# Optimization experiments

Hardware: AMD Instinct MI355X
Metric: run time of the kernel (lower is better)

## Reference

```python
import jax, jax.numpy as jnp
import numpy as np

BS, LS, NWRD, D, H, NTGT, MC = 32, 512, 100000, 128, 512, 2048, 20
TEMP = 0.5  # gumbel-softmax temperature (self.last_t)
HLOSS_COEF = 0.03


def setup_inputs() -> dict:
    key = jax.random.key(0)
    ks = jax.random.split(key, 12)
    inp_word = jax.random.randint(ks[0], (BS, LS), 0, NWRD, dtype=jnp.int32)
    inp_char = jax.random.randint(ks[1], (BS, LS, MC), 0, 95, dtype=jnp.int32)
    inp_pos = jax.random.randint(ks[2], (BS, LS), 0, 50, dtype=jnp.int32)
    keyword_table = jax.random.bernoulli(ks[3], 0.1, (NWRD,))  # wid in keywords_set
    tgt_ids = jax.random.randint(ks[4], (NTGT,), 0, NWRD, dtype=jnp.int32)
    lut = jax.random.randint(ks[5], (NWRD, MC), 0, 95, dtype=jnp.int32)
    u = jax.random.uniform(ks[6], (BS, LS, NTGT), minval=1e-6, maxval=1.0 - 1e-6)
    gumbel = -jnp.log(-jnp.log(u))  # standard Gumbel(0,1) noise
    W = jax.random.normal(ks[7], (NWRD, D), dtype=jnp.float32) * 0.02
    W1 = jax.random.normal(ks[8], (D, H), dtype=jnp.float32) * (1.0 / np.sqrt(D))
    b1 = jnp.zeros((H,), jnp.float32)
    W2 = jax.random.normal(ks[9], (H, NTGT), dtype=jnp.float32) * (1.0 / np.sqrt(H))
    b2 = jnp.zeros((NTGT,), jnp.float32)
    return dict(inp_word=inp_word, inp_char=inp_char, inp_pos=inp_pos,
                keyword_table=keyword_table, tgt_ids=tgt_ids, lut=lut,
                gumbel=gumbel, W=W, W1=W1, b1=b1, W2=W2, b2=b2)


def reference(inp_word, inp_char, inp_pos, keyword_table, tgt_ids, lut,
              gumbel, W, W1, b1, W2, b2):
    # keyword membership mask (idx in the original; torch gathers only masked
    # spots -- here we compute densely and select with the mask, same math at
    # every masked position, identity elsewhere)
    mask = keyword_table[inp_word]                      # [bs, ls] bool

    x = W[inp_word]                                     # embed: [bs, ls, d]
    hdn = jax.nn.relu(jnp.einsum('bsd,dh->bsh', x, W1) + b1)
    logits = jnp.einsum('bsh,ht->bst', hdn, W2) + b2    # [bs, ls, ntgt]

    # log_p.masked_scatter_(idx, x.max(-1)[0])
    log_p = jnp.where(mask, logits.max(axis=-1), 0.0)

    # hloss: mean entropy over masked spots * 0.03
    lsm = jax.nn.log_softmax(logits, axis=-1)
    ent = -jnp.sum(jnp.exp(lsm) * lsm, axis=-1)         # [bs, ls]
    n_spots = jnp.maximum(mask.sum(), 1)
    loss_h = (ent * mask).sum() / n_spots * HLOSS_COEF

    # gumbel_softmax(x, t): softmax((logits + g) / t)
    sft = jax.nn.softmax((logits + gumbel) / TEMP, axis=-1)  # [bs, ls, ntgt]

    # hard pick mapped through tgtwords, scattered into word
    y = tgt_ids[jnp.argmax(sft, axis=-1)]               # [bs, ls]
    word = jnp.where(mask, y, inp_word)

    # soft embedding: sft @ word_emb_tgt, word_emb_tgt = W[tgt_ids]
    x_emb = jnp.einsum('bst,td->bsd', sft, W[tgt_ids])  # [bs, ls, d]
    word_emb = jnp.where(mask[..., None], x_emb, x)     # scatter into W[word]

    char = lut[word]                                    # word_to_char lookup

    return (mask.astype(jnp.float32), log_p, word, char, word_emb, loss_h)
```

## Files before the change

kernel.cpp:

```cpp
#include <hip/hip_runtime.h>
#include <cstdint>

#define R_TOT 16384
#define T_NT  2048
#define DD    128
#define HH    512
#define MC_   20
#define BR    32
#define STEPS 64
#define NBLK  (R_TOT / BR)

#define MASK_OFF 0
#define LOGP_OFF 16384
#define WORD_OFF 32768
#define CHAR_OFF 49152
#define EMB_OFF  376832
#define LOSS_OFF 2473984

#define X_OFF     0
#define HDN_OFF   2097152
#define HDNB_OFF  10485760
#define WT_OFF    14680064
#define WTT4_OFF  14942208
#define W2T_OFF   15204352
#define W2P_OFF   16252928
#define ENT_OFF   16777216
#define CNT_OFF   16777728

typedef __attribute__((ext_vector_type(8))) short short8v;
typedef __attribute__((ext_vector_type(4))) float f32x4;
typedef unsigned short ushort_t;

__device__ __forceinline__ ushort_t f2bf(float f) {
    union { float f; unsigned int u; } v; v.f = f;
    unsigned int r = v.u + 0x7FFFu + ((v.u >> 16) & 1u);
    return (ushort_t)(r >> 16);
}

__device__ __forceinline__ void stage16(const ushort_t* gsrc, ushort_t* ldst) {
    __builtin_amdgcn_global_load_lds(
        (const __attribute__((address_space(1))) unsigned int*)gsrc,
        (__attribute__((address_space(3))) unsigned int*)ldst, 16, 0, 0);
}

__global__ __launch_bounds__(256) void k1_gather(
    const int* __restrict__ inp_word, const int* __restrict__ tgt_ids,
    const float* __restrict__ W, float* __restrict__ x, float* __restrict__ wtgt)
{
    int row = blockIdx.x * 2 + (threadIdx.x >> 7);
    int d = threadIdx.x & 127;
    if (row < R_TOT) {
        int wsrc = inp_word[row];
        x[(size_t)row * DD + d] = W[(size_t)wsrc * DD + d];
    } else {
        int rr = row - R_TOT;
        if (rr < T_NT) {
            int wsrc = tgt_ids[rr];
            wtgt[(size_t)rr * DD + d] = W[(size_t)wsrc * DD + d];
        }
    }
}

__global__ __launch_bounds__(256) void k1b_wtgtT4(
    const float* __restrict__ wtgt, ushort_t* __restrict__ wtgtT4)
{
    const int js = blockIdx.x, t = threadIdx.x;
    #pragma unroll
    for (int i = 0; i < 4; ++i) {
        int s = i * 256 + t;
        int cs = s >> 9, rem = s & 511;
        int df = rem >> 6, lane = rem & 63;
        int lrow = lane & 15, kg = lane >> 4;
        ushort_t* dst = wtgtT4 + (size_t)(((js * 2 + cs) * 8 + df) * 512 + lane * 8);
        #pragma unroll
        for (int j = 0; j < 8; ++j) {
            dst[j] = (j < 4)
                ? f2bf(wtgt[(size_t)(js * 32 + cs * 16 + kg * 4 + j) * DD + df * 16 + lrow])
                : (ushort_t)0;
        }
    }
}

__global__ __launch_bounds__(256) void k0_w2t(
    const float* __restrict__ W2, float* __restrict__ W2Tf, ushort_t* __restrict__ W2p)
{
    __shared__ float tile[32][33];
    const int js = blockIdx.x, ks = blockIdx.y;
    const int cb = js * 32, kb = ks * 32;
    const int lx = threadIdx.x & 31, ly = threadIdx.x >> 5;
    #pragma unroll
    for (int i = 0; i < 32; i += 8)
        tile[ly + i][lx] = W2[(size_t)(kb + ly + i) * T_NT + cb + lx];
    __syncthreads();
    #pragma unroll
    for (int i = 0; i < 32; i += 8) {
        int c = cb + ly + i, k = kb + lx;
        W2Tf[(size_t)c * HH + k] = tile[lx][ly + i];
    }
    if (threadIdx.x < 128) {
        int c = threadIdx.x >> 2, kgrp = threadIdx.x & 3;
        ushort_t* dst = W2p + (size_t)((js * 16 + ks) * 1024 + (c * 4 + kgrp) * 8);
        #pragma unroll
        for (int i = 0; i < 8; ++i)
            dst[i] = f2bf(tile[kgrp * 8 + i][c]);
    }
}

__global__ __launch_bounds__(256) void k2_hdn(
    const float* __restrict__ x, const float* __restrict__ W1,
    const float* __restrict__ b1, float* __restrict__ hdn, ushort_t* __restrict__ hdnB)
{
    __shared__ float As[16][64];
    __shared__ float Bs[16][64];
    const int t = threadIdx.x;
    const int bm = blockIdx.x * 64;
    const int bn = blockIdx.y * 64;
    const int tx = t & 15, ty = t >> 4;
    float acc[4][4] = {};
    for (int k0 = 0; k0 < DD; k0 += 16) {
        {
            int m = t >> 2, kq = t & 3;
            float4 v = *(const float4*)(x + (size_t)(bm + m) * DD + k0 + kq * 4);
            As[kq * 4 + 0][m] = v.x; As[kq * 4 + 1][m] = v.y;
            As[kq * 4 + 2][m] = v.z; As[kq * 4 + 3][m] = v.w;
        }
        {
            int k = t >> 4, nq = t & 15;
            *(float4*)(&Bs[k][nq * 4]) =
                *(const float4*)(W1 + (size_t)(k0 + k) * HH + bn + nq * 4);
        }
        __syncthreads();
        #pragma unroll
        for (int k = 0; k < 16; ++k) {
            float a[4], b[4];
            #pragma unroll
            for (int i = 0; i < 4; i++) a[i] = As[k][ty * 4 + i];
            #pragma unroll
            for (int j = 0; j < 4; j++) b[j] = Bs[k][tx * 4 + j];
            #pragma unroll
            for (int i = 0; i < 4; i++)
                #pragma unroll
                for (int j = 0; j < 4; j++)
                    acc[i][j] = fmaf(a[i], b[j], acc[i][j]);
        }
        __syncthreads();
    }
    #pragma unroll
    for (int i = 0; i < 4; i++) {
        int m = bm + ty * 4 + i;
        int n = bn + tx * 4;
        float4 v;
        v.x = fmaxf(acc[i][0] + b1[n + 0], 0.f);
        v.y = fmaxf(acc[i][1] + b1[n + 1], 0.f);
        v.z = fmaxf(acc[i][2] + b1[n + 2], 0.f);
        v.w = fmaxf(acc[i][3] + b1[n + 3], 0.f);
        *(float4*)(hdn + (size_t)m * HH + n) = v;
        ushort4 hb;
        hb.x = f2bf(v.x); hb.y = f2bf(v.y); hb.z = f2bf(v.z); hb.w = f2bf(v.w);
        *(ushort4*)(hdnB + (size_t)m * HH + n) = hb;
    }
}

__global__ __launch_bounds__(256) void k3_fused(
    const ushort_t* __restrict__ hdnB, const float* __restrict__ hdn,
    const ushort_t* __restrict__ W2p, const float* __restrict__ W2Tf,
    const float* __restrict__ b2, const float* __restrict__ gumbel,
    const int* __restrict__ inp_word, const int* __restrict__ keyword_table,
    const int* __restrict__ tgt_ids, const int* __restrict__ lut,
    const float* __restrict__ x, const ushort_t* __restrict__ wtgtT4,
    float* __restrict__ out, float* __restrict__ entP, float* __restrict__ cntP)
{
    __shared__ ushort_t wS[2 * 16384];
    __shared__ float statC1[32 * 8];
    __shared__ int   candS[BR * 2];
    __shared__ float invs2S[BR], entS[BR];
    __shared__ int   mskS[BR];

    const int t = threadIdx.x;
    const int wid = t >> 6, lane = t & 63;
    const int Mgrp = wid >> 1, Cgrp = wid & 1;
    const int lrow = lane & 15, kgrp = lane >> 4;
    const int row0 = blockIdx.x * BR;
    const int rowA = row0 + Mgrp * 16 + lrow;

    short8v av[16];
    #pragma unroll
    for (int ks = 0; ks < 16; ++ks)
        av[ks] = *(const short8v*)(hdnB + (size_t)rowA * HH + ks * 32 + kgrp * 8);

    const ushort_t* wb = wS + ((Cgrp * 16 + lrow) * 4 + kgrp) * 8;

    const float* gp = gumbel + (size_t)rowA * T_NT + Cgrp * 16 + kgrp * 4;
    const float* b2p = b2 + Cgrp * 16 + kgrp * 4;
    const ushort_t* vtp = wtgtT4 + (size_t)Cgrp * 4096 + lane * 8;

    float m_ = -1e30f, sE_ = 0.f, sEl_ = 0.f, s2_ = 0.f;
    float a1_ = -1e30f, a2_ = -1e30f;
    int i1_ = 0, i2_ = 0;
    f32x4 accpv[8];
    #pragma unroll
    for (int df = 0; df < 8; ++df) accpv[df] = (f32x4){0.f, 0.f, 0.f, 0.f};

    {
        const ushort_t* src = W2p + t * 8;
        ushort_t* dst = wS + t * 8;
        #pragma unroll
        for (int i = 0; i < 8; ++i) stage16(src + i * 2048, dst + i * 2048);
    }
    float4 g4 = *(const float4*)gp;
    float4 b2v4 = *(const float4*)b2p;
    __syncthreads();

    int c0 = Cgrp * 16 + kgrp * 4;

    for (int s = 0; s < STEPS; ++s) {
        const int buf = s & 1;

        if (s + 1 < STEPS) {
            const ushort_t* src = W2p + (size_t)(s + 1) * 16384 + t * 8;
            ushort_t* dst = wS + (buf ^ 1) * 16384 + t * 8;
            #pragma unroll
            for (int i = 0; i < 8; ++i) stage16(src + i * 2048, dst + i * 2048);
        }
        const int adv = (s + 1 < STEPS) ? 32 : 0;
        float4 gn4 = *(const float4*)(gp + adv);
        float4 b2n4 = *(const float4*)(b2p + adv);
        gp += 32; b2p += 32;
        short8v bvf[8];
        #pragma unroll
        for (int df = 0; df < 8; ++df)
            bvf[df] = *(const short8v*)(vtp + df * 512);
        vtp += 8192;

        const ushort_t* wbb = wb + buf * 16384;
        f32x4 ac0 = (f32x4){0.f,0.f,0.f,0.f}, ac1 = ac0, ac2 = ac0, ac3 = ac0;
        #pragma unroll
        for (int ks = 0; ks < 16; ks += 4) {
            ac0 = __builtin_amdgcn_mfma_f32_16x16x32_bf16(*(const short8v*)(wbb + (ks+0)*1024), av[ks+0], ac0, 0, 0, 0);
            ac1 = __builtin_amdgcn_mfma_f32_16x16x32_bf16(*(const short8v*)(wbb + (ks+1)*1024), av[ks+1], ac1, 0, 0, 0);
            ac2 = __builtin_amdgcn_mfma_f32_16x16x32_bf16(*(const short8v*)(wbb + (ks+2)*1024), av[ks+2], ac2, 0, 0, 0);
            ac3 = __builtin_amdgcn_mfma_f32_16x16x32_bf16(*(const short8v*)(wbb + (ks+3)*1024), av[ks+3], ac3, 0, 0, 0);
        }
        f32x4 acc = (ac0 + ac1) + (ac2 + ac3);

        short8v pav;
        pav[4] = 0; pav[5] = 0; pav[6] = 0; pav[7] = 0;
        #pragma unroll
        for (int q = 0; q < 4; ++q) {
            float l = acc[q] + b2v4[q];
            m_ = fmaxf(m_, l);
            float e1 = __expf(l);
            sE_ += e1; sEl_ = fmaf(e1, l, sEl_);
            float a = l + g4[q];
            float p = __expf(2.0f * a);
            s2_ += p;
            if (a > a1_) { a2_ = a1_; i2_ = i1_; a1_ = a; i1_ = c0 + q; }
            else if (a > a2_) { a2_ = a; i2_ = c0 + q; }
            pav[q] = (short)f2bf(p);
        }

        #pragma unroll
        for (int df = 0; df < 8; ++df)
            accpv[df] = __builtin_amdgcn_mfma_f32_16x16x32_bf16(pav, bvf[df], accpv[df], 0, 0, 0);

        g4 = gn4; b2v4 = b2n4; c0 += 32;
        __syncthreads();
    }

    #pragma unroll
    for (int mk = 16; mk < 64; mk <<= 1) {
        m_ = fmaxf(m_, __shfl_xor(m_, mk));
        sE_ += __shfl_xor(sE_, mk);
        sEl_ += __shfl_xor(sEl_, mk);
        s2_ += __shfl_xor(s2_, mk);
        float ob1 = __shfl_xor(a1_, mk); int oj1 = __shfl_xor(i1_, mk);
        float ob2 = __shfl_xor(a2_, mk); int oj2 = __shfl_xor(i2_, mk);
        if (ob1 > a1_ || (ob1 == a1_ && oj1 < i1_)) {
            if (a1_ > ob2 || (a1_ == ob2 && i1_ < oj2)) { a2_ = a1_; i2_ = i1_; }
            else { a2_ = ob2; i2_ = oj2; }
            a1_ = ob1; i1_ = oj1;
        } else {
            if (ob1 > a2_) { a2_ = ob1; i2_ = oj1; }
        }
    }

    if (Cgrp == 1 && lane < 16) {
        float* st = &statC1[(Mgrp * 16 + lane) * 8];
        st[0] = m_; st[1] = sE_; st[2] = sEl_; st[3] = s2_;
        st[4] = a1_; st[5] = __int_as_float(i1_);
        st[6] = a2_; st[7] = __int_as_float(i2_);
    }
    float* scr = (float*)wS;
    if (Cgrp == 1) {
        #pragma unroll
        for (int df = 0; df < 8; ++df)
            #pragma unroll
            for (int q = 0; q < 4; ++q)
                scr[Mgrp * 2048 + (kgrp * 4 + q) * 128 + df * 16 + lrow] = accpv[df][q];
    }
    __syncthreads();

    if (Cgrp == 0) {
        if (lane < 16) {
            const float* st = &statC1[(Mgrp * 16 + lane) * 8];
            float bm = st[0], bsE = st[1], bsEl = st[2], bs2 = st[3];
            float ob1 = st[4]; int oj1 = __float_as_int(st[5]);
            float ob2 = st[6]; int oj2 = __float_as_int(st[7]);
            float m = fmaxf(m_, bm);
            float sE = sE_ + bsE, sEl = sEl_ + bsEl, s2 = s2_ + bs2;
            float a1 = a1_, a2 = a2_; int i1 = i1_, i2 = i2_;
            if (ob1 > a1 || (ob1 == a1 && oj1 < i1)) {
                if (a1 > ob2 || (a1 == ob2 && i1 < oj2)) { a2 = a1; i2 = i1; }
                else { a2 = ob2; i2 = oj2; }
                a1 = ob1; i1 = oj1;
            } else {
                if (ob1 > a2) { a2 = ob1; i2 = oj1; }
            }
            int rl = Mgrp * 16 + lane;
            int grow = row0 + rl;
            int w_in = inp_word[grow];
            int msk = keyword_table[w_in] != 0;
            out[MASK_OFF + grow] = msk ? 1.0f : 0.0f;
            out[LOGP_OFF + grow] = msk ? m : 0.0f;
            invs2S[rl] = 1.0f / s2;
            mskS[rl] = msk;
            entS[rl] = msk ? (__logf(sE) - sEl / sE) : 0.0f;
            candS[rl * 2 + 0] = i1;
            candS[rl * 2 + 1] = i2;
        }
        #pragma unroll
        for (int df = 0; df < 8; ++df)
            #pragma unroll
            for (int q = 0; q < 4; ++q)
                accpv[df][q] += scr[Mgrp * 2048 + (kgrp * 4 + q) * 128 + df * 16 + lrow];
    }
    __syncthreads();

    if (Cgrp == 0) {
        #pragma unroll
        for (int df = 0; df < 8; ++df) {
            #pragma unroll
            for (int q = 0; q < 4; ++q) {
                int rl = Mgrp * 16 + kgrp * 4 + q;
                int grow = row0 + rl;
                int d = df * 16 + lrow;
                float val = accpv[df][q] * invs2S[rl];
                if (!mskS[rl]) val = x[(size_t)grow * DD + d];
                out[EMB_OFF + (size_t)grow * DD + d] = val;
            }
        }
    }

    for (int rr = wid; rr < BR; rr += 4) {
        int grow = row0 + rr;
        int i1 = candS[rr * 2 + 0], i2 = candS[rr * 2 + 1];
        const float* hrow = hdn + (size_t)grow * HH;
        float4 h0 = *(const float4*)(hrow + lane * 8);
        float4 h1 = *(const float4*)(hrow + lane * 8 + 4);
        float v1, v2;
        {
            const float* wrow = W2Tf + (size_t)i1 * HH;
            float4 w0 = *(const float4*)(wrow + lane * 8);
            float4 w1 = *(const float4*)(wrow + lane * 8 + 4);
            float sdot = h0.x*w0.x + h0.y*w0.y + h0.z*w0.z + h0.w*w0.w
                       + h1.x*w1.x + h1.y*w1.y + h1.z*w1.z + h1.w*w1.w;
            #pragma unroll
            for (int mk = 1; mk < 64; mk <<= 1) sdot += __shfl_xor(sdot, mk);
            v1 = sdot + b2[i1] + gumbel[(size_t)grow * T_NT + i1];
        }
        {
            const float* wrow = W2Tf + (size_t)i2 * HH;
            float4 w0 = *(const float4*)(wrow + lane * 8);
            float4 w1 = *(const float4*)(wrow + lane * 8 + 4);
            float sdot = h0.x*w0.x + h0.y*w0.y + h0.z*w0.z + h0.w*w0.w
                       + h1.x*w1.x + h1.y*w1.y + h1.z*w1.z + h1.w*w1.w;
            #pragma unroll
            for (int mk = 1; mk < 64; mk <<= 1) sdot += __shfl_xor(sdot, mk);
            v2 = sdot + b2[i2] + gumbel[(size_t)grow * T_NT + i2];
        }
        int ibest = (v2 > v1 || (v2 == v1 && i2 < i1)) ? i2 : i1;
        int w_in = inp_word[grow];
        int msk = mskS[rr];
        int word = msk ? tgt_ids[ibest] : w_in;
        if (lane == 0) out[WORD_OFF + grow] = (float)word;
        if (lane < MC_)
            out[CHAR_OFF + (size_t)grow * MC_ + lane] = (float)lut[(size_t)word * MC_ + lane];
    }

    if (t == 0) {
        float es = 0.f; int cs = 0;
        #pragma unroll
        for (int r = 0; r < BR; r++) { es += entS[r]; cs += mskS[r]; }
        entP[blockIdx.x] = es;
        cntP[blockIdx.x] = (float)cs;
    }
}

__global__ __launch_bounds__(256) void k4_loss(
    const float* __restrict__ entP, const float* __restrict__ cntP, float* __restrict__ out)
{
    __shared__ float sE[256], sC[256];
    int t = threadIdx.x;
    float e = 0.f, c = 0.f;
    for (int i = t; i < NBLK; i += 256) { e += entP[i]; c += cntP[i]; }
    sE[t] = e; sC[t] = c;
    __syncthreads();
    for (int s = 128; s > 0; s >>= 1) {
        if (t < s) { sE[t] += sE[t + s]; sC[t] += sC[t + s]; }
        __syncthreads();
    }
    if (t == 0) {
        float ns = fmaxf(sC[0], 1.0f);
        out[LOSS_OFF] = 0.03f * sE[0] / ns;
    }
}

extern "C" void kernel_launch(void* const* d_in, const int* in_sizes, int n_in,
                              void* d_out, int out_size, void* d_ws, size_t ws_size,
                              hipStream_t stream) {
    const int* inp_word = (const int*)d_in[0];
    const int* keyword_table = (const int*)d_in[3];
    const int* tgt_ids = (const int*)d_in[4];
    const int* lut = (const int*)d_in[5];
    const float* gumbel = (const float*)d_in[6];
    const float* W = (const float*)d_in[7];
    const float* W1 = (const float*)d_in[8];
    const float* b1 = (const float*)d_in[9];
    const float* W2 = (const float*)d_in[10];
    const float* b2 = (const float*)d_in[11];
    float* out = (float*)d_out;

    float* wsf = (float*)d_ws;
    float* x = wsf + X_OFF;
    float* hdn = wsf + HDN_OFF;
    ushort_t* hdnB = (ushort_t*)(wsf + HDNB_OFF);
    float* wtgt = wsf + WT_OFF;
    ushort_t* wtgtT4 = (ushort_t*)(wsf + WTT4_OFF);
    float* W2Tf = wsf + W2T_OFF;
    ushort_t* W2p = (ushort_t*)(wsf + W2P_OFF);
    float* entP = wsf + ENT_OFF;
    float* cntP = wsf + CNT_OFF;

    k1_gather<<<(R_TOT + T_NT) / 2, 256, 0, stream>>>(inp_word, tgt_ids, W, x, wtgt);
    k1b_wtgtT4<<<64, 256, 0, stream>>>(wtgt, wtgtT4);
    k0_w2t<<<dim3(T_NT / 32, HH / 32), 256, 0, stream>>>(W2, W2Tf, W2p);
    k2_hdn<<<dim3(R_TOT / 64, HH / 64), 256, 0, stream>>>(x, W1, b1, hdn, hdnB);
    k3_fused<<<NBLK, 256, 0, stream>>>(hdnB, hdn, W2p, W2Tf, b2, gumbel,
                                       inp_word, keyword_table, tgt_ids, lut,
                                       x, wtgtT4, out, entP, cntP);
    k4_loss<<<1, 256, 0, stream>>>(entP, cntP, out);
}
```

Baseline: 206.2 us.

## Triple-buffer W2 tiles in half-K chunks and relayout packed W2 for LDS reads

Splits each 32-column W2 step into two half-K chunks of 8192 elements and cycles them through a three-slot LDS ring instead of a two-slot double buffer. This cuts k3 shared memory from 64KB to 48KB, which may allow more resident blocks, and issues each prefetch earlier relative to use. The packed W2 layout is changed from (c,kgrp) to (kgrp,c) interleaving, with read offsets to match, so that LDS reads are contiguous across lanes. It adds a second barrier per step and more index bookkeeping.

```diff
diff --git a/kernel.cpp b/kernel.cpp
--- a/kernel.cpp
+++ b/kernel.cpp
@@ -99,7 +99,7 @@
     }
     if (threadIdx.x < 128) {
         int c = threadIdx.x >> 2, kgrp = threadIdx.x & 3;
-        ushort_t* dst = W2p + (size_t)((js * 16 + ks) * 1024 + (c * 4 + kgrp) * 8);
+        ushort_t* dst = W2p + (size_t)((js * 16 + ks) * 1024 + (kgrp * 32 + c) * 8);
         #pragma unroll
         for (int i = 0; i < 8; ++i)
             dst[i] = f2bf(tile[kgrp * 8 + i][c]);
@@ -170,7 +170,7 @@
     const float* __restrict__ x, const ushort_t* __restrict__ wtgtT4,
     float* __restrict__ out, float* __restrict__ entP, float* __restrict__ cntP)
 {
-    __shared__ ushort_t wS[2 * 16384];
+    __shared__ ushort_t wS3[3 * 8192];
     __shared__ float statC1[32 * 8];
     __shared__ int   candS[BR * 2];
     __shared__ float invs2S[BR], entS[BR];
@@ -188,7 +188,8 @@
     for (int ks = 0; ks < 16; ++ks)
         av[ks] = *(const short8v*)(hdnB + (size_t)rowA * HH + ks * 32 + kgrp * 8);
 
-    const ushort_t* wb = wS + ((Cgrp * 16 + lrow) * 4 + kgrp) * 8;
+    const int rdoff = (kgrp * 32 + Cgrp * 16 + lrow) * 8;
+    const int stoff = t * 8;
 
     const float* gp = gumbel + (size_t)rowA * T_NT + Cgrp * 16 + kgrp * 4;
     const float* b2p = b2 + Cgrp * 16 + kgrp * 4;
@@ -202,26 +203,42 @@
     for (int df = 0; df < 8; ++df) accpv[df] = (f32x4){0.f, 0.f, 0.f, 0.f};
 
     {
-        const ushort_t* src = W2p + t * 8;
-        ushort_t* dst = wS + t * 8;
-        #pragma unroll
-        for (int i = 0; i < 8; ++i) stage16(src + i * 2048, dst + i * 2048);
+        const ushort_t* sp = W2p + stoff;
+        #pragma unroll
+        for (int i = 0; i < 4; ++i) stage16(sp + i * 2048, wS3 + stoff + i * 2048);
+        #pragma unroll
+        for (int i = 0; i < 4; ++i) stage16(sp + 8192 + i * 2048, wS3 + 8192 + stoff + i * 2048);
     }
     float4 g4 = *(const float4*)gp;
     float4 b2v4 = *(const float4*)b2p;
     __syncthreads();
 
+    const ushort_t* spT = W2p + 16384 + stoff;
+    int offC = 0, offN = 8192, offS = 16384;
     int c0 = Cgrp * 16 + kgrp * 4;
 
     for (int s = 0; s < STEPS; ++s) {
-        const int buf = s & 1;
-
-        if (s + 1 < STEPS) {
-            const ushort_t* src = W2p + (size_t)(s + 1) * 16384 + t * 8;
-            ushort_t* dst = wS + (buf ^ 1) * 16384 + t * 8;
-            #pragma unroll
-            for (int i = 0; i < 8; ++i) stage16(src + i * 2048, dst + i * 2048);
-        }
+        f32x4 ac0 = (f32x4){0.f,0.f,0.f,0.f}, ac1 = ac0, ac2 = ac0, ac3 = ac0;
+        {
+            const ushort_t* cr = wS3 + offC + rdoff;
+            #pragma unroll
+            for (int ksl = 0; ksl < 8; ksl += 4) {
+                ac0 = __builtin_amdgcn_mfma_f32_16x16x32_bf16(*(const short8v*)(cr + (ksl+0)*1024), av[ksl+0], ac0, 0, 0, 0);
+                ac1 = __builtin_amdgcn_mfma_f32_16x16x32_bf16(*(const short8v*)(cr + (ksl+1)*1024), av[ksl+1], ac1, 0, 0, 0);
+                ac2 = __builtin_amdgcn_mfma_f32_16x16x32_bf16(*(const short8v*)(cr + (ksl+2)*1024), av[ksl+2], ac2, 0, 0, 0);
+                ac3 = __builtin_amdgcn_mfma_f32_16x16x32_bf16(*(const short8v*)(cr + (ksl+3)*1024), av[ksl+3], ac3, 0, 0, 0);
+            }
+        }
+        __syncthreads();
+
+        if (2 * s + 2 < 2 * STEPS) {
+            ushort_t* dst = wS3 + offS + stoff;
+            #pragma unroll
+            for (int i = 0; i < 4; ++i) stage16(spT + i * 2048, dst + i * 2048);
+            spT += 8192;
+        }
+        { int tmp = offC; offC = offN; offN = offS; offS = tmp; }
+
         const int adv = (s + 1 < STEPS) ? 32 : 0;
         float4 gn4 = *(const float4*)(gp + adv);
         float4 b2n4 = *(const float4*)(b2p + adv);
@@ -232,14 +249,15 @@
             bvf[df] = *(const short8v*)(vtp + df * 512);
         vtp += 8192;
 
-        const ushort_t* wbb = wb + buf * 16384;
-        f32x4 ac0 = (f32x4){0.f,0.f,0.f,0.f}, ac1 = ac0, ac2 = ac0, ac3 = ac0;
-        #pragma unroll
-        for (int ks = 0; ks < 16; ks += 4) {
-            ac0 = __builtin_amdgcn_mfma_f32_16x16x32_bf16(*(const short8v*)(wbb + (ks+0)*1024), av[ks+0], ac0, 0, 0, 0);
-            ac1 = __builtin_amdgcn_mfma_f32_16x16x32_bf16(*(const short8v*)(wbb + (ks+1)*1024), av[ks+1], ac1, 0, 0, 0);
-            ac2 = __builtin_amdgcn_mfma_f32_16x16x32_bf16(*(const short8v*)(wbb + (ks+2)*1024), av[ks+2], ac2, 0, 0, 0);
-            ac3 = __builtin_amdgcn_mfma_f32_16x16x32_bf16(*(const short8v*)(wbb + (ks+3)*1024), av[ks+3], ac3, 0, 0, 0);
+        {
+            const ushort_t* cr = wS3 + offC + rdoff;
+            #pragma unroll
+            for (int ksl = 0; ksl < 8; ksl += 4) {
+                ac0 = __builtin_amdgcn_mfma_f32_16x16x32_bf16(*(const short8v*)(cr + (ksl+0)*1024), av[8+ksl+0], ac0, 0, 0, 0);
+                ac1 = __builtin_amdgcn_mfma_f32_16x16x32_bf16(*(const short8v*)(cr + (ksl+1)*1024), av[8+ksl+1], ac1, 0, 0, 0);
+                ac2 = __builtin_amdgcn_mfma_f32_16x16x32_bf16(*(const short8v*)(cr + (ksl+2)*1024), av[8+ksl+2], ac2, 0, 0, 0);
+                ac3 = __builtin_amdgcn_mfma_f32_16x16x32_bf16(*(const short8v*)(cr + (ksl+3)*1024), av[8+ksl+3], ac3, 0, 0, 0);
+            }
         }
         f32x4 acc = (ac0 + ac1) + (ac2 + ac3);
 
@@ -265,6 +283,14 @@
 
         g4 = gn4; b2v4 = b2n4; c0 += 32;
         __syncthreads();
+
+        if (2 * s + 3 < 2 * STEPS) {
+            ushort_t* dst = wS3 + offS + stoff;
+            #pragma unroll
+            for (int i = 0; i < 4; ++i) stage16(spT + i * 2048, dst + i * 2048);
+            spT += 8192;
+        }
+        { int tmp = offC; offC = offN; offN = offS; offS = tmp; }
     }
 
     #pragma unroll
@@ -290,7 +316,7 @@
         st[4] = a1_; st[5] = __int_as_float(i1_);
         st[6] = a2_; st[7] = __int_as_float(i2_);
     }
-    float* scr = (float*)wS;
+    float* scr = (float*)wS3;
     if (Cgrp == 1) {
         #pragma unroll
         for (int df = 0; df < 8; ++df)
```

After: 199.5 us. 3.2% less time.

## Restructure fused logits kernel: 16-row blocks, wave-split column chunks, direct global W2 reads

Applied to the files above, without the earlier changes.

The fused projection/softmax kernel now handles 16 rows per block (1024 blocks) instead of 32. Each of the 4 waves owns a disjoint, rotated quarter of the 2048 target columns, reading W2 fragments straight from global/L2 in a new packed layout instead of double-buffering them through LDS with global_load_lds and per-step barriers. The soft-embedding B operand is repacked so all 8 bf16 slots are used, halving the wasted MFMA work on the P·V product. A 4-way cross-wave merge of softmax statistics and partial accumulators replaces the old 2-way merge. The aim is to remove per-step synchronisation and raise parallelism, at the cost of more L2 traffic for W2 since each block re-reads all of W2 for half as many rows.

```diff
diff --git a/kernel.cpp b/kernel.cpp
--- a/kernel.cpp
+++ b/kernel.cpp
@@ -6,9 +6,9 @@
 #define DD    128
 #define HH    512
 #define MC_   20
-#define BR    32
-#define STEPS 64
-#define NBLK  (R_TOT / BR)
+#define BR    16
+#define NBLK  1024
+#define SPW   16
 
 #define MASK_OFF 0
 #define LOGP_OFF 16384
@@ -21,11 +21,11 @@
 #define HDN_OFF   2097152
 #define HDNB_OFF  10485760
 #define WT_OFF    14680064
-#define WTT4_OFF  14942208
+#define WTT5_OFF  14942208
 #define W2T_OFF   15204352
-#define W2P_OFF   16252928
+#define W2Q_OFF   16252928
 #define ENT_OFF   16777216
-#define CNT_OFF   16777728
+#define CNT_OFF   16778240
 
 typedef __attribute__((ext_vector_type(8))) short short8v;
 typedef __attribute__((ext_vector_type(4))) float f32x4;
@@ -35,12 +35,6 @@
     union { float f; unsigned int u; } v; v.f = f;
     unsigned int r = v.u + 0x7FFFu + ((v.u >> 16) & 1u);
     return (ushort_t)(r >> 16);
-}
-
-__device__ __forceinline__ void stage16(const ushort_t* gsrc, ushort_t* ldst) {
-    __builtin_amdgcn_global_load_lds(
-        (const __attribute__((address_space(1))) unsigned int*)gsrc,
-        (__attribute__((address_space(3))) unsigned int*)ldst, 16, 0, 0);
 }
 
 __global__ __launch_bounds__(256) void k1_gather(
@@ -61,28 +55,26 @@
     }
 }
 
-__global__ __launch_bounds__(256) void k1b_wtgtT4(
-    const float* __restrict__ wtgt, ushort_t* __restrict__ wtgtT4)
-{
-    const int js = blockIdx.x, t = threadIdx.x;
-    #pragma unroll
-    for (int i = 0; i < 4; ++i) {
-        int s = i * 256 + t;
-        int cs = s >> 9, rem = s & 511;
-        int df = rem >> 6, lane = rem & 63;
+__global__ __launch_bounds__(256) void k1b_wtgtT5(
+    const float* __restrict__ wtgt, ushort_t* __restrict__ wtgtT5)
+{
+    const int sc = blockIdx.x, t = threadIdx.x;
+    #pragma unroll
+    for (int it = 0; it < 2; ++it) {
+        int idx = it * 256 + t;
+        int df = idx >> 6, lane = idx & 63;
         int lrow = lane & 15, kg = lane >> 4;
-        ushort_t* dst = wtgtT4 + (size_t)(((js * 2 + cs) * 8 + df) * 512 + lane * 8);
+        ushort_t* dst = wtgtT5 + ((size_t)sc * 8 + df) * 512 + lane * 8;
         #pragma unroll
         for (int j = 0; j < 8; ++j) {
-            dst[j] = (j < 4)
-                ? f2bf(wtgt[(size_t)(js * 32 + cs * 16 + kg * 4 + j) * DD + df * 16 + lrow])
-                : (ushort_t)0;
+            int col = sc * 32 + (j < 4 ? kg * 4 + j : 16 + kg * 4 + (j - 4));
+            dst[j] = f2bf(wtgt[(size_t)col * DD + df * 16 + lrow]);
         }
     }
 }
 
 __global__ __launch_bounds__(256) void k0_w2t(
-    const float* __restrict__ W2, float* __restrict__ W2Tf, ushort_t* __restrict__ W2p)
+    const float* __restrict__ W2, float* __restrict__ W2Tf, ushort_t* __restrict__ W2q)
 {
     __shared__ float tile[32][33];
     const int js = blockIdx.x, ks = blockIdx.y;
@@ -99,7 +91,8 @@
     }
     if (threadIdx.x < 128) {
         int c = threadIdx.x >> 2, kgrp = threadIdx.x & 3;
-        ushort_t* dst = W2p + (size_t)((js * 16 + ks) * 1024 + (c * 4 + kgrp) * 8);
+        int cs = c >> 4, lrow = c & 15;
+        ushort_t* dst = W2q + (size_t)(((js * 2 + cs) * 16 + ks) * 512) + (kgrp * 16 + lrow) * 8;
         #pragma unroll
         for (int i = 0; i < 8; ++i)
             dst[i] = f2bf(tile[kgrp * 8 + i][c]);
@@ -163,36 +156,41 @@
 
 __global__ __launch_bounds__(256) void k3_fused(
     const ushort_t* __restrict__ hdnB, const float* __restrict__ hdn,
-    const ushort_t* __restrict__ W2p, const float* __restrict__ W2Tf,
+    const ushort_t* __restrict__ W2q, const float* __restrict__ W2Tf,
     const float* __restrict__ b2, const float* __restrict__ gumbel,
     const int* __restrict__ inp_word, const int* __restrict__ keyword_table,
     const int* __restrict__ tgt_ids, const int* __restrict__ lut,
-    const float* __restrict__ x, const ushort_t* __restrict__ wtgtT4,
+    const float* __restrict__ x, const ushort_t* __restrict__ wtgtT5,
     float* __restrict__ out, float* __restrict__ entP, float* __restrict__ cntP)
 {
-    __shared__ ushort_t wS[2 * 16384];
-    __shared__ float statC1[32 * 8];
+    __shared__ float bigS[6144];
+    __shared__ float statP[4][16][8];
     __shared__ int   candS[BR * 2];
     __shared__ float invs2S[BR], entS[BR];
     __shared__ int   mskS[BR];
 
     const int t = threadIdx.x;
     const int wid = t >> 6, lane = t & 63;
-    const int Mgrp = wid >> 1, Cgrp = wid & 1;
     const int lrow = lane & 15, kgrp = lane >> 4;
     const int row0 = blockIdx.x * BR;
-    const int rowA = row0 + Mgrp * 16 + lrow;
-
-    short8v av[16];
-    #pragma unroll
-    for (int ks = 0; ks < 16; ++ks)
-        av[ks] = *(const short8v*)(hdnB + (size_t)rowA * HH + ks * 32 + kgrp * 8);
-
-    const ushort_t* wb = wS + ((Cgrp * 16 + lrow) * 4 + kgrp) * 8;
-
-    const float* gp = gumbel + (size_t)rowA * T_NT + Cgrp * 16 + kgrp * 4;
-    const float* b2p = b2 + Cgrp * 16 + kgrp * 4;
-    const ushort_t* vtp = wtgtT4 + (size_t)Cgrp * 4096 + lane * 8;
+
+    ushort_t* aP = (ushort_t*)bigS;
+
+    #pragma unroll
+    for (int it = 0; it < 4; ++it) {
+        int gid = it * 256 + t;
+        int ks = gid >> 6, l2 = gid & 63;
+        int lr = l2 & 15, kg = l2 >> 4;
+        uint4 v = *(const uint4*)(hdnB + (size_t)(row0 + lr) * HH + ks * 32 + kg * 8);
+        *(uint4*)(aP + gid * 8) = v;
+    }
+    __syncthreads();
+
+    const int scq = (int)((blockIdx.x + wid) & 3);
+    const int srot = (int)((blockIdx.x >> 2) & 15);
+
+    const ushort_t* aRd = aP + lane * 8;
+    const float* gRow = gumbel + (size_t)(row0 + lrow) * T_NT + kgrp * 4;
 
     float m_ = -1e30f, sE_ = 0.f, sEl_ = 0.f, s2_ = 0.f;
     float a1_ = -1e30f, a2_ = -1e30f;
@@ -202,69 +200,75 @@
     for (int df = 0; df < 8; ++df) accpv[df] = (f32x4){0.f, 0.f, 0.f, 0.f};
 
     {
-        const ushort_t* src = W2p + t * 8;
-        ushort_t* dst = wS + t * 8;
-        #pragma unroll
-        for (int i = 0; i < 8; ++i) stage16(src + i * 2048, dst + i * 2048);
-    }
-    float4 g4 = *(const float4*)gp;
-    float4 b2v4 = *(const float4*)b2p;
-    __syncthreads();
-
-    int c0 = Cgrp * 16 + kgrp * 4;
-
-    for (int s = 0; s < STEPS; ++s) {
-        const int buf = s & 1;
-
-        if (s + 1 < STEPS) {
-            const ushort_t* src = W2p + (size_t)(s + 1) * 16384 + t * 8;
-            ushort_t* dst = wS + (buf ^ 1) * 16384 + t * 8;
-            #pragma unroll
-            for (int i = 0; i < 8; ++i) stage16(src + i * 2048, dst + i * 2048);
-        }
-        const int adv = (s + 1 < STEPS) ? 32 : 0;
-        float4 gn4 = *(const float4*)(gp + adv);
-        float4 b2n4 = *(const float4*)(b2p + adv);
-        gp += 32; b2p += 32;
-        short8v bvf[8];
-        #pragma unroll
-        for (int df = 0; df < 8; ++df)
-            bvf[df] = *(const short8v*)(vtp + df * 512);
-        vtp += 8192;
-
-        const ushort_t* wbb = wb + buf * 16384;
-        f32x4 ac0 = (f32x4){0.f,0.f,0.f,0.f}, ac1 = ac0, ac2 = ac0, ac3 = ac0;
-        #pragma unroll
-        for (int ks = 0; ks < 16; ks += 4) {
-            ac0 = __builtin_amdgcn_mfma_f32_16x16x32_bf16(*(const short8v*)(wbb + (ks+0)*1024), av[ks+0], ac0, 0, 0, 0);
-            ac1 = __builtin_amdgcn_mfma_f32_16x16x32_bf16(*(const short8v*)(wbb + (ks+1)*1024), av[ks+1], ac1, 0, 0, 0);
-            ac2 = __builtin_amdgcn_mfma_f32_16x16x32_bf16(*(const short8v*)(wbb + (ks+2)*1024), av[ks+2], ac2, 0, 0, 0);
-            ac3 = __builtin_amdgcn_mfma_f32_16x16x32_bf16(*(const short8v*)(wbb + (ks+3)*1024), av[ks+3], ac3, 0, 0, 0);
-        }
-        f32x4 acc = (ac0 + ac1) + (ac2 + ac3);
+        int sc00 = scq + 4 * (srot & 15);
+    }
+    f32x4 ga, gb;
+    {
+        int sc00 = scq + 4 * (srot & 15);
+        ga = *(const f32x4*)(gRow + sc00 * 32);
+        gb = *(const f32x4*)(gRow + sc00 * 32 + 16);
+    }
+
+    for (int s = 0; s < SPW; ++s) {
+        const int sc = scq + 4 * ((s + srot) & 15);
+        const int scn = scq + 4 * ((s + 1 + srot) & 15);
+
+        f32x4 gna = *(const f32x4*)(gRow + scn * 32);
+        f32x4 gnb = *(const f32x4*)(gRow + scn * 32 + 16);
+
+        f32x4 b2a = *(const f32x4*)(b2 + sc * 32 + kgrp * 4);
+        f32x4 b2b = *(const f32x4*)(b2 + sc * 32 + kgrp * 4 + 16);
+
+        const ushort_t* w2a = W2q + (size_t)sc * 16384 + lane * 8;
+        f32x4 c0[4], c1[4];
+        #pragma unroll
+        for (int j = 0; j < 4; ++j) { c0[j] = (f32x4){0.f,0.f,0.f,0.f}; c1[j] = c0[j]; }
+        #pragma unroll
+        for (int ks = 0; ks < 16; ++ks) {
+            short8v avk = *(const short8v*)(aRd + ks * 512);
+            short8v wa0 = *(const short8v*)(w2a + ks * 512);
+            short8v wa1 = *(const short8v*)(w2a + 8192 + ks * 512);
+            c0[ks & 3] = __builtin_amdgcn_mfma_f32_16x16x32_bf16(wa0, avk, c0[ks & 3], 0, 0, 0);
+            c1[ks & 3] = __builtin_amdgcn_mfma_f32_16x16x32_bf16(wa1, avk, c1[ks & 3], 0, 0, 0);
+        }
+        f32x4 acc0 = (c0[0] + c0[1]) + (c0[2] + c0[3]);
+        f32x4 acc1 = (c1[0] + c1[1]) + (c1[2] + c1[3]);
 
         short8v pav;
-        pav[4] = 0; pav[5] = 0; pav[6] = 0; pav[7] = 0;
+        const int colb = sc * 32 + kgrp * 4;
         #pragma unroll
         for (int q = 0; q < 4; ++q) {
-            float l = acc[q] + b2v4[q];
-            m_ = fmaxf(m_, l);
-            float e1 = __expf(l);
-            sE_ += e1; sEl_ = fmaf(e1, l, sEl_);
-            float a = l + g4[q];
-            float p = __expf(2.0f * a);
-            s2_ += p;
-            if (a > a1_) { a2_ = a1_; i2_ = i1_; a1_ = a; i1_ = c0 + q; }
-            else if (a > a2_) { a2_ = a; i2_ = c0 + q; }
-            pav[q] = (short)f2bf(p);
-        }
-
-        #pragma unroll
-        for (int df = 0; df < 8; ++df)
-            accpv[df] = __builtin_amdgcn_mfma_f32_16x16x32_bf16(pav, bvf[df], accpv[df], 0, 0, 0);
-
-        g4 = gn4; b2v4 = b2n4; c0 += 32;
-        __syncthreads();
+            float l0 = acc0[q] + b2a[q];
+            m_ = fmaxf(m_, l0);
+            float e0 = __expf(l0);
+            sE_ += e0; sEl_ = fmaf(e0, l0, sEl_);
+            float aa0 = l0 + ga[q];
+            float p0 = __expf(2.0f * aa0);
+            s2_ += p0;
+            if (aa0 > a1_) { a2_ = a1_; i2_ = i1_; a1_ = aa0; i1_ = colb + q; }
+            else if (aa0 > a2_) { a2_ = aa0; i2_ = colb + q; }
+            pav[q] = (short)f2bf(p0);
+
+            float l1 = acc1[q] + b2b[q];
+            m_ = fmaxf(m_, l1);
+            float e1 = __expf(l1);
+            sE_ += e1; sEl_ = fmaf(e1, l1, sEl_);
+            float aa1 = l1 + gb[q];
+            float p1 = __expf(2.0f * aa1);
+            s2_ += p1;
+            if (aa1 > a1_) { a2_ = a1_; i2_ = i1_; a1_ = aa1; i1_ = colb + 16 + q; }
+            else if (aa1 > a2_) { a2_ = aa1; i2_ = colb + 16 + q; }
+            pav[4 + q] = (short)f2bf(p1);
+        }
+
+        const ushort_t* vt = wtgtT5 + (size_t)sc * 4096 + lane * 8;
+        #pragma unroll
+        for (int df = 0; df < 8; ++df) {
+            short8v bv = *(const short8v*)(vt + df * 512);
+            accpv[df] = __builtin_amdgcn_mfma_f32_16x16x32_bf16(pav, bv, accpv[df], 0, 0, 0);
+        }
+
+        ga = gna; gb = gnb;
     }
 
     #pragma unroll
@@ -284,64 +288,69 @@
         }
     }
 
-    if (Cgrp == 1 && lane < 16) {
-        float* st = &statC1[(Mgrp * 16 + lane) * 8];
+    __syncthreads();
+
+    if (lane < 16) {
+        float* st = &statP[wid][lane][0];
         st[0] = m_; st[1] = sE_; st[2] = sEl_; st[3] = s2_;
         st[4] = a1_; st[5] = __int_as_float(i1_);
         st[6] = a2_; st[7] = __int_as_float(i2_);
     }
-    float* scr = (float*)wS;
-    if (Cgrp == 1) {
+    if (wid >= 1) {
+        float* scr = bigS + (wid - 1) * 2048;
         #pragma unroll
         for (int df = 0; df < 8; ++df)
             #pragma unroll
             for (int q = 0; q < 4; ++q)
-                scr[Mgrp * 2048 + (kgrp * 4 + q) * 128 + df * 16 + lrow] = accpv[df][q];
-    }
-    __syncthreads();
-
-    if (Cgrp == 0) {
+                scr[(kgrp * 4 + q) * 128 + df * 16 + lrow] = accpv[df][q];
+    }
+    __syncthreads();
+
+    if (wid == 0) {
         if (lane < 16) {
-            const float* st = &statC1[(Mgrp * 16 + lane) * 8];
-            float bm = st[0], bsE = st[1], bsEl = st[2], bs2 = st[3];
-            float ob1 = st[4]; int oj1 = __float_as_int(st[5]);
-            float ob2 = st[6]; int oj2 = __float_as_int(st[7]);
-            float m = fmaxf(m_, bm);
-            float sE = sE_ + bsE, sEl = sEl_ + bsEl, s2 = s2_ + bs2;
-            float a1 = a1_, a2 = a2_; int i1 = i1_, i2 = i2_;
-            if (ob1 > a1 || (ob1 == a1 && oj1 < i1)) {
-                if (a1 > ob2 || (a1 == ob2 && i1 < oj2)) { a2 = a1; i2 = i1; }
-                else { a2 = ob2; i2 = oj2; }
-                a1 = ob1; i1 = oj1;
-            } else {
-                if (ob1 > a2) { a2 = ob1; i2 = oj1; }
+            float M = -1e30f, SE = 0.f, SEL = 0.f, S2 = 0.f;
+            float A1 = -1e30f, A2 = -1e30f; int I1 = 0, I2 = 0;
+            #pragma unroll
+            for (int w = 0; w < 4; ++w) {
+                const float* st = &statP[w][lane][0];
+                float ob1 = st[4]; int oj1 = __float_as_int(st[5]);
+                float ob2 = st[6]; int oj2 = __float_as_int(st[7]);
+                M = fmaxf(M, st[0]); SE += st[1]; SEL += st[2]; S2 += st[3];
+                if (ob1 > A1 || (ob1 == A1 && oj1 < I1)) {
+                    if (A1 > ob2 || (A1 == ob2 && I1 < oj2)) { A2 = A1; I2 = I1; }
+                    else { A2 = ob2; I2 = oj2; }
+                    A1 = ob1; I1 = oj1;
+                } else {
+                    if (ob1 > A2) { A2 = ob1; I2 = oj1; }
+                }
             }
-            int rl = Mgrp * 16 + lane;
-            int grow = row0 + rl;
+            int grow = row0 + lane;
             int w_in = inp_word[grow];
             int msk = keyword_table[w_in] != 0;
             out[MASK_OFF + grow] = msk ? 1.0f : 0.0f;
-            out[LOGP_OFF + grow] = msk ? m : 0.0f;
-            invs2S[rl] = 1.0f / s2;
-            mskS[rl] = msk;
-            entS[rl] = msk ? (__logf(sE) - sEl / sE) : 0.0f;
-            candS[rl * 2 + 0] = i1;
-            candS[rl * 2 + 1] = i2;
+            out[LOGP_OFF + grow] = msk ? M : 0.0f;
+            invs2S[lane] = 1.0f / S2;
+            mskS[lane] = msk;
+            entS[lane] = msk ? (__logf(SE) - SEL / SE) : 0.0f;
+            candS[lane * 2 + 0] = I1;
+            candS[lane * 2 + 1] = I2;
         }
         #pragma unroll
         for (int df = 0; df < 8; ++df)
             #pragma unroll
             for (int q = 0; q < 4; ++q)
-                accpv[df][q] += scr[Mgrp * 2048 + (kgrp * 4 + q) * 128 + df * 16 + lrow];
-    }
-    __syncthreads();
-
-    if (Cgrp == 0) {
+                accpv[df][q] += bigS[0 * 2048 + (kgrp * 4 + q) * 128 + df * 16 + lrow]
+                              + bigS[1 * 2048 + (kgrp * 4 + q) * 128 + df * 16 + lrow]
+                              + bigS[2 * 2048 + (kgrp * 4 + q) * 128 + df * 16 + lrow];
+    }
+    __syncthreads();
+
+    if (wid == 0) {
         #pragma unroll
         for (int df = 0; df < 8; ++df) {
             #pragma unroll
             for (int q = 0; q < 4; ++q) {
-                int rl = Mgrp * 16 + kgrp * 4 + q;
+                int rl = kgrp * 4 + q;
                 int grow = row0 + rl;
                 int d = df * 16 + lrow;
                 float val = accpv[df][q] * invs2S[rl];
@@ -354,6 +363,7 @@
     for (int rr = wid; rr < BR; rr += 4) {
         int grow = row0 + rr;
         int i1 = candS[rr * 2 + 0], i2 = candS[rr * 2 + 1];
+        int mskr = mskS[rr];
         const float* hrow = hdn + (size_t)grow * HH;
         float4 h0 = *(const float4*)(hrow + lane * 8);
         float4 h1 = *(const float4*)(hrow + lane * 8 + 4);
@@ -379,9 +389,7 @@
             v2 = sdot + b2[i2] + gumbel[(size_t)grow * T_NT + i2];
         }
         int ibest = (v2 > v1 || (v2 == v1 && i2 < i1)) ? i2 : i1;
-        int w_in = inp_word[grow];
-        int msk = mskS[rr];
-        int word = msk ? tgt_ids[ibest] : w_in;
+        int word = mskr ? tgt_ids[ibest] : inp_word[grow];
         if (lane == 0) out[WORD_OFF + grow] = (float)word;
         if (lane < MC_)
             out[CHAR_OFF + (size_t)grow * MC_ + lane] = (float)lut[(size_t)word * MC_ + lane];
@@ -435,18 +443,18 @@
     float* hdn = wsf + HDN_OFF;
     ushort_t* hdnB = (ushort_t*)(wsf + HDNB_OFF);
     float* wtgt = wsf + WT_OFF;
-    ushort_t* wtgtT4 = (ushort_t*)(wsf + WTT4_OFF);
+    ushort_t* wtgtT5 = (ushort_t*)(wsf + WTT5_OFF);
     float* W2Tf = wsf + W2T_OFF;
-    ushort_t* W2p = (ushort_t*)(wsf + W2P_OFF);
+    ushort_t* W2q = (ushort_t*)(wsf + W2Q_OFF);
     float* entP = wsf + ENT_OFF;
     float* cntP = wsf + CNT_OFF;
 
     k1_gather<<<(R_TOT + T_NT) / 2, 256, 0, stream>>>(inp_word, tgt_ids, W, x, wtgt);
-    k1b_wtgtT4<<<64, 256, 0, stream>>>(wtgt, wtgtT4);
-    k0_w2t<<<dim3(T_NT / 32, HH / 32), 256, 0, stream>>>(W2, W2Tf, W2p);
+    k1b_wtgtT5<<<64, 256, 0, stream>>>(wtgt, wtgtT5);
+    k0_w2t<<<dim3(T_NT / 32, HH / 32), 256, 0, stream>>>(W2, W2Tf, W2q);
     k2_hdn<<<dim3(R_TOT / 64, HH / 64), 256, 0, stream>>>(x, W1, b1, hdn, hdnB);
-    k3_fused<<<NBLK, 256, 0, stream>>>(hdnB, hdn, W2p, W2Tf, b2, gumbel,
+    k3_fused<<<NBLK, 256, 0, stream>>>(hdnB, hdn, W2q, W2Tf, b2, gumbel,
                                        inp_word, keyword_table, tgt_ids, lut,
-                                       x, wtgtT4, out, entP, cntP);
+                                       x, wtgtT5, out, entP, cntP);
     k4_loss<<<1, 256, 0, stream>>>(entP, cntP, out);
 }
```

After: 238.3 us. 1.16x slower.
